# Kernel optimization log

Hardware: AMD Instinct MI355X
Metric: run time of the kernel (lower is better)

The kernel has to match this reference:

```python
import jax, jax.numpy as jnp
import numpy as np

NUM_RADIAL = 8    # radial Gaussian shells
NUM_ANGULAR = 4   # l=0 (scalar) + l=1 (unit direction x,y,z)
MAX_R = 3.0       # max radius covered by radial basis
GAMMA = 8.0       # Gaussian sharpness ~ (NUM_RADIAL/MAX_R)^2
C_IN = 16
C_OUT = 16
EPS = 1e-12


def setup_inputs() -> dict:
    key = jax.random.key(0)
    k1, k2, k3 = jax.random.split(key, 3)
    features = jax.random.normal(k1, (4, 512, C_IN), dtype=jnp.float32)
    geometry = jax.random.normal(k2, (4, 512, 3), dtype=jnp.float32)
    # learned kernel weights mixing radial x angular basis into [out,in] channel map
    W = jax.random.normal(k3, (NUM_RADIAL, NUM_ANGULAR, C_OUT, C_IN), dtype=jnp.float32)
    W = W / np.float32(np.sqrt(NUM_RADIAL * NUM_ANGULAR * C_IN))
    return {"features": features, "geometry": geometry, "W": W, "n_norm": 512}


def _kernel_basis(rel):
    # rel: [z, a, b, 3] relative positions (r_b - r_a)
    d = jnp.sqrt(jnp.sum(rel * rel, axis=-1) + EPS)           # [z,a,b]
    unit = rel / d[..., None]                                  # [z,a,b,3]
    # angular basis: l=0 constant + l=1 unit vector -> [z,a,b,4]
    ang = jnp.concatenate([jnp.ones_like(d)[..., None], unit], axis=-1)
    centers = jnp.linspace(0.0, MAX_R, NUM_RADIAL, dtype=rel.dtype)
    rad = jnp.exp(-GAMMA * (d[..., None] - centers) ** 2)      # [z,a,b,R]
    return rad, ang


def reference(features, geometry, W, n_norm):
    # rb - ra with out_geometry = geometry (module default)
    rel = geometry[:, None, :, :] - geometry[:, :, None, :]    # [z,a,b,3]
    rad, ang = _kernel_basis(rel)
    # dense pairwise kernel [z,a,b,i,j] (this is the HBM-heavy intermediate)
    k = jnp.einsum('zabr,zabm,rmij->zabij', rad, ang, W)
    k = k * (1.0 / jnp.sqrt(jnp.asarray(n_norm, dtype=features.dtype)))
    # contract kernel with input features over neighbor b and in-channel j
    return jnp.einsum('zabij,zbj->zai', k, features)
```

## Files before the change

kernel.cpp:

```cpp
#include <hip/hip_runtime.h>
#include <hip/hip_fp16.h>

typedef _Float16 f16x8 __attribute__((ext_vector_type(8)));
typedef float    f32x4 __attribute__((ext_vector_type(4)));

#define S    512
#define CIN  16
#define COUT 16

static __device__ inline unsigned int pkrtz(float lo, float hi) {
    auto h = __builtin_amdgcn_cvt_pkrtz(lo, hi);
    return __builtin_bit_cast(unsigned int, h);
}

__global__ __launch_bounds__(256, 2)
void econv_mfma(const float* __restrict__ feat,
                const float* __restrict__ geom,
                const float* __restrict__ Wm,
                const int*   __restrict__ n_norm,
                float*       __restrict__ out)
{
    __shared__ float          Glds[S * 3];
    __shared__ unsigned short FtU[16 * S];
    __shared__ unsigned short BasU[4 * 32 * 128];

    const int t = threadIdx.x;
    const int z = blockIdx.x >> 7;
    const int a0 = (blockIdx.x & 127) << 2;
    const int w = t >> 6;
    const int l = t & 63;

    const float* gz = geom + z * S * 3;
    const float* fz = feat + z * S * CIN;

    for (int k = t; k < S * 3; k += 256) Glds[k] = gz[k];

    {
        const int j  = t & 15;
        const int b0 = (t >> 4) * 32;
        const int key = (j & 7) << 4;
        char* FtB = (char*)FtU;
#pragma unroll
        for (int bi = 0; bi < 32; bi += 2) {
            float f0 = fz[(b0 + bi) * CIN + j];
            float f1 = fz[(b0 + bi + 1) * CIN + j];
            *(unsigned int*)(FtB + j * 1024 + ((2 * (b0 + bi)) ^ key)) = pkrtz(f0, f1);
        }
    }
    __syncthreads();

    const int a = a0 + w;
    const float gax = Glds[3 * a], gay = Glds[3 * a + 1], gaz = Glds[3 * a + 2];

    char* BasB = (char*)(BasU + w * 32 * 128);
    char* FtB  = (char*)FtU;

    const int mrow = l & 15;
    const int g    = l >> 4;
    const int rkey = (mrow & 7) << 4;
    const int wbase = 4 * l;

    f32x4 acc0 = {0.f, 0.f, 0.f, 0.f};
    f32x4 acc1 = {0.f, 0.f, 0.f, 0.f};

    for (int c = 0; c < 4; ++c) {
        float v0[32];
        unsigned int pw[32];
        {
            const int b = c * 128 + 2 * l;
            float dx = Glds[3 * b] - gax, dy = Glds[3 * b + 1] - gay, dz = Glds[3 * b + 2] - gaz;
            float ss  = fmaf(dx, dx, fmaf(dy, dy, fmaf(dz, dz, 1e-12f)));
            float inv = rsqrtf(ss);
            float d   = ss * inv;
            float ux = dx * inv, uy = dy * inv, uz = dz * inv;
#pragma unroll
            for (int r = 0; r < 8; ++r) {
                float e   = d - (float)r * (3.0f / 7.0f);
                float rad = __expf(-8.0f * e * e);
                v0[4 * r]     = rad;
                v0[4 * r + 1] = rad * ux;
                v0[4 * r + 2] = rad * uy;
                v0[4 * r + 3] = rad * uz;
            }
        }
        {
            const int b = c * 128 + 2 * l + 1;
            float dx = Glds[3 * b] - gax, dy = Glds[3 * b + 1] - gay, dz = Glds[3 * b + 2] - gaz;
            float ss  = fmaf(dx, dx, fmaf(dy, dy, fmaf(dz, dz, 1e-12f)));
            float inv = rsqrtf(ss);
            float d   = ss * inv;
            float ux = dx * inv, uy = dy * inv, uz = dz * inv;
#pragma unroll
            for (int r = 0; r < 8; ++r) {
                float e   = d - (float)r * (3.0f / 7.0f);
                float rad = __expf(-8.0f * e * e);
                pw[4 * r]     = pkrtz(v0[4 * r],     rad);
                pw[4 * r + 1] = pkrtz(v0[4 * r + 1], rad * ux);
                pw[4 * r + 2] = pkrtz(v0[4 * r + 2], rad * uy);
                pw[4 * r + 3] = pkrtz(v0[4 * r + 3], rad * uz);
            }
        }
#pragma unroll
        for (int rm = 0; rm < 32; ++rm) {
            *(unsigned int*)(BasB + rm * 256 + (wbase ^ ((rm & 7) << 4))) = pw[rm];
        }

#pragma unroll
        for (int ks = 0; ks < 4; ++ks) {
            const int colb = 64 * ks + 16 * g;
            f16x8 A0 = *(f16x8*)(BasB + mrow * 256        + (colb ^ rkey));
            f16x8 A1 = *(f16x8*)(BasB + (mrow + 16) * 256 + (colb ^ rkey));
            f16x8 Bf = *(f16x8*)(FtB  + mrow * 1024 + ((c * 256 + colb) ^ rkey));
            acc0 = __builtin_amdgcn_mfma_f32_16x16x32_f16(A0, Bf, acc0, 0, 0, 0);
            acc1 = __builtin_amdgcn_mfma_f32_16x16x32_f16(A1, Bf, acc1, 0, 0, 0);
        }
    }

    float* Tl = (float*)BasB;
#pragma unroll
    for (int q = 0; q < 4; ++q) {
        Tl[(4 * g + q) * 16 + mrow]      = acc0[q];
        Tl[(16 + 4 * g + q) * 16 + mrow] = acc1[q];
    }

    float o = 0.f;
    const float* Wp = Wm + (g * 8) * COUT * CIN + mrow * CIN;
#pragma unroll
    for (int rr = 0; rr < 8; ++rr) {
        const float* Trow = Tl + (g * 8 + rr) * 16;
        const float* Wrow = Wp + rr * COUT * CIN;
#pragma unroll
        for (int j4 = 0; j4 < 4; ++j4) {
            f32x4 tv = *(const f32x4*)(Trow + 4 * j4);
            f32x4 wv = *(const f32x4*)(Wrow + 4 * j4);
            o = fmaf(tv[0], wv[0], o);
            o = fmaf(tv[1], wv[1], o);
            o = fmaf(tv[2], wv[2], o);
            o = fmaf(tv[3], wv[3], o);
        }
    }
    o += __shfl_xor(o, 16);
    o += __shfl_xor(o, 32);
    if (l < 16) {
        const float scale = rsqrtf((float)n_norm[0]);
        out[(z * S + a) * COUT + mrow] = o * scale;
    }
}

extern "C" void kernel_launch(void* const* d_in, const int* in_sizes, int n_in,
                              void* d_out, int out_size, void* d_ws, size_t ws_size,
                              hipStream_t stream) {
    const float* feat   = (const float*)d_in[0];
    const float* geomp  = (const float*)d_in[1];
    const float* Wm     = (const float*)d_in[2];
    const int*   n_norm = (const int*)d_in[3];
    float* outp = (float*)d_out;

    dim3 grid(512), block(256);
    econv_mfma<<<grid, block, 0, stream>>>(feat, geomp, Wm, n_norm, outp);
}
```

Before: 14.93 us.

## Split each atom's neighbor range across two waves and double the grid

```diff
diff --git a/kernel.cpp b/kernel.cpp
--- a/kernel.cpp
+++ b/kernel.cpp
@@ -13,7 +13,7 @@
     return __builtin_bit_cast(unsigned int, h);
 }
 
-__global__ __launch_bounds__(256, 2)
+__global__ __launch_bounds__(256, 4)
 void econv_mfma(const float* __restrict__ feat,
                 const float* __restrict__ geom,
                 const float* __restrict__ Wm,
@@ -22,18 +22,22 @@
 {
     __shared__ float          Glds[S * 3];
     __shared__ unsigned short FtU[16 * S];
-    __shared__ unsigned short BasU[4 * 32 * 128];
+    __shared__ unsigned short BasU[4 * 32 * 64];
 
     const int t = threadIdx.x;
-    const int z = blockIdx.x >> 7;
-    const int a0 = (blockIdx.x & 127) << 2;
+    const int z = blockIdx.x >> 8;
+    const int a0 = (blockIdx.x & 255) << 1;
     const int w = t >> 6;
     const int l = t & 63;
+    const int a_loc = w >> 1;
+    const int wh    = w & 1;
 
     const float* gz = geom + z * S * 3;
     const float* fz = feat + z * S * CIN;
 
-    for (int k = t; k < S * 3; k += 256) Glds[k] = gz[k];
+#pragma unroll
+    for (int k = 0; k < (S * 3) / 256; ++k)
+        Glds[k * 256 + t] = gz[k * 256 + t];
 
     {
         const int j  = t & 15;
@@ -49,68 +53,63 @@
     }
     __syncthreads();
 
-    const int a = a0 + w;
+    const int a = a0 + a_loc;
     const float gax = Glds[3 * a], gay = Glds[3 * a + 1], gaz = Glds[3 * a + 2];
 
-    char* BasB = (char*)(BasU + w * 32 * 128);
+    char* BasB = (char*)(BasU + w * 32 * 64);
     char* FtB  = (char*)FtU;
 
     const int mrow = l & 15;
     const int g    = l >> 4;
     const int rkey = (mrow & 7) << 4;
-    const int wbase = 4 * l;
+    const int s    = l & 31;
+    const int hh   = l >> 5;
 
     f32x4 acc0 = {0.f, 0.f, 0.f, 0.f};
     f32x4 acc1 = {0.f, 0.f, 0.f, 0.f};
 
     for (int c = 0; c < 4; ++c) {
-        float v0[32];
-        unsigned int pw[32];
-        {
-            const int b = c * 128 + 2 * l;
-            float dx = Glds[3 * b] - gax, dy = Glds[3 * b + 1] - gay, dz = Glds[3 * b + 2] - gaz;
-            float ss  = fmaf(dx, dx, fmaf(dy, dy, fmaf(dz, dz, 1e-12f)));
-            float inv = rsqrtf(ss);
-            float d   = ss * inv;
-            float ux = dx * inv, uy = dy * inv, uz = dz * inv;
+        const int bloc = wh * 256 + c * 64 + 2 * s;
+        const char* gp = (const char*)Glds + 12 * bloc;
+        float2 g01 = *(const float2*)(gp);
+        float2 g23 = *(const float2*)(gp + 8);
+        float2 g45 = *(const float2*)(gp + 16);
+
+        float dx0 = g01.x - gax, dy0 = g01.y - gay, dz0 = g23.x - gaz;
+        float dx1 = g23.y - gax, dy1 = g45.x - gay, dz1 = g45.y - gaz;
+        float ss0 = fmaf(dx0, dx0, fmaf(dy0, dy0, fmaf(dz0, dz0, 1e-12f)));
+        float ss1 = fmaf(dx1, dx1, fmaf(dy1, dy1, fmaf(dz1, dz1, 1e-12f)));
+        float inv0 = rsqrtf(ss0), inv1 = rsqrtf(ss1);
+        float dd0 = ss0 * inv0,  dd1 = ss1 * inv1;
+        float ux0 = dx0 * inv0, uy0 = dy0 * inv0, uz0 = dz0 * inv0;
+        float ux1 = dx1 * inv1, uy1 = dy1 * inv1, uz1 = dz1 * inv1;
+
+        unsigned int pw[16];
 #pragma unroll
-            for (int r = 0; r < 8; ++r) {
-                float e   = d - (float)r * (3.0f / 7.0f);
-                float rad = __expf(-8.0f * e * e);
-                v0[4 * r]     = rad;
-                v0[4 * r + 1] = rad * ux;
-                v0[4 * r + 2] = rad * uy;
-                v0[4 * r + 3] = rad * uz;
-            }
+        for (int rr = 0; rr < 4; ++rr) {
+            const float cen = (float)(4 * hh + rr) * (3.0f / 7.0f);
+            float e0 = dd0 - cen, e1 = dd1 - cen;
+            float rad0 = __expf(-8.0f * e0 * e0);
+            float rad1 = __expf(-8.0f * e1 * e1);
+            pw[4 * rr + 0] = pkrtz(rad0,       rad1);
+            pw[4 * rr + 1] = pkrtz(rad0 * ux0, rad1 * ux1);
+            pw[4 * rr + 2] = pkrtz(rad0 * uy0, rad1 * uy1);
+            pw[4 * rr + 3] = pkrtz(rad0 * uz0, rad1 * uz1);
         }
-        {
-            const int b = c * 128 + 2 * l + 1;
-            float dx = Glds[3 * b] - gax, dy = Glds[3 * b + 1] - gay, dz = Glds[3 * b + 2] - gaz;
-            float ss  = fmaf(dx, dx, fmaf(dy, dy, fmaf(dz, dz, 1e-12f)));
-            float inv = rsqrtf(ss);
-            float d   = ss * inv;
-            float ux = dx * inv, uy = dy * inv, uz = dz * inv;
+        const unsigned int wb = 4 * s;
 #pragma unroll
-            for (int r = 0; r < 8; ++r) {
-                float e   = d - (float)r * (3.0f / 7.0f);
-                float rad = __expf(-8.0f * e * e);
-                pw[4 * r]     = pkrtz(v0[4 * r],     rad);
-                pw[4 * r + 1] = pkrtz(v0[4 * r + 1], rad * ux);
-                pw[4 * r + 2] = pkrtz(v0[4 * r + 2], rad * uy);
-                pw[4 * r + 3] = pkrtz(v0[4 * r + 3], rad * uz);
-            }
-        }
-#pragma unroll
-        for (int rm = 0; rm < 32; ++rm) {
-            *(unsigned int*)(BasB + rm * 256 + (wbase ^ ((rm & 7) << 4))) = pw[rm];
+        for (int k = 0; k < 16; ++k) {
+            const int rm = hh * 16 + k;
+            *(unsigned int*)(BasB + rm * 128 + (wb ^ ((k & 7) << 4))) = pw[k];
         }
 
 #pragma unroll
-        for (int ks = 0; ks < 4; ++ks) {
+        for (int ks = 0; ks < 2; ++ks) {
             const int colb = 64 * ks + 16 * g;
-            f16x8 A0 = *(f16x8*)(BasB + mrow * 256        + (colb ^ rkey));
-            f16x8 A1 = *(f16x8*)(BasB + (mrow + 16) * 256 + (colb ^ rkey));
-            f16x8 Bf = *(f16x8*)(FtB  + mrow * 1024 + ((c * 256 + colb) ^ rkey));
+            f16x8 A0 = *(f16x8*)(BasB + mrow * 128        + (colb ^ rkey));
+            f16x8 A1 = *(f16x8*)(BasB + (mrow + 16) * 128 + (colb ^ rkey));
+            f16x8 Bf = *(f16x8*)(FtB + mrow * 1024 +
+                                 ((wh * 512 + c * 128 + colb) ^ rkey));
             acc0 = __builtin_amdgcn_mfma_f32_16x16x32_f16(A0, Bf, acc0, 0, 0, 0);
             acc1 = __builtin_amdgcn_mfma_f32_16x16x32_f16(A1, Bf, acc1, 0, 0, 0);
         }
@@ -122,28 +121,32 @@
         Tl[(4 * g + q) * 16 + mrow]      = acc0[q];
         Tl[(16 + 4 * g + q) * 16 + mrow] = acc1[q];
     }
+    __syncthreads();
 
-    float o = 0.f;
-    const float* Wp = Wm + (g * 8) * COUT * CIN + mrow * CIN;
+    if (wh == 0) {
+        const float* T0 = (const float*)((const char*)BasU + (2 * a_loc)     * 4096);
+        const float* T1 = (const float*)((const char*)BasU + (2 * a_loc + 1) * 4096);
+        float o = 0.f;
 #pragma unroll
-    for (int rr = 0; rr < 8; ++rr) {
-        const float* Trow = Tl + (g * 8 + rr) * 16;
-        const float* Wrow = Wp + rr * COUT * CIN;
+        for (int rr = 0; rr < 8; ++rr) {
+            const int row = g * 8 + rr;
 #pragma unroll
-        for (int j4 = 0; j4 < 4; ++j4) {
-            f32x4 tv = *(const f32x4*)(Trow + 4 * j4);
-            f32x4 wv = *(const f32x4*)(Wrow + 4 * j4);
-            o = fmaf(tv[0], wv[0], o);
-            o = fmaf(tv[1], wv[1], o);
-            o = fmaf(tv[2], wv[2], o);
-            o = fmaf(tv[3], wv[3], o);
+            for (int j4 = 0; j4 < 4; ++j4) {
+                f32x4 tv = *(const f32x4*)(T0 + row * 16 + 4 * j4) +
+                           *(const f32x4*)(T1 + row * 16 + 4 * j4);
+                f32x4 wv = *(const f32x4*)(Wm + row * 256 + mrow * 16 + 4 * j4);
+                o = fmaf(tv[0], wv[0], o);
+                o = fmaf(tv[1], wv[1], o);
+                o = fmaf(tv[2], wv[2], o);
+                o = fmaf(tv[3], wv[3], o);
+            }
         }
-    }
-    o += __shfl_xor(o, 16);
-    o += __shfl_xor(o, 32);
-    if (l < 16) {
-        const float scale = rsqrtf((float)n_norm[0]);
-        out[(z * S + a) * COUT + mrow] = o * scale;
+        o += __shfl_xor(o, 16);
+        o += __shfl_xor(o, 32);
+        if (l < 16) {
+            const float scale = rsqrtf((float)n_norm[0]);
+            out[(z * S + a) * COUT + mrow] = o * scale;
+        }
     }
 }
 
@@ -156,6 +159,6 @@
     const int*   n_norm = (const int*)d_in[3];
     float* outp = (float*)d_out;
 
-    dim3 grid(512), block(256);
+    dim3 grid(1024), block(256);
     econv_mfma<<<grid, block, 0, stream>>>(feat, geomp, Wm, n_norm, outp);
 }
```

After: 15.84 us. 1.06x slower.

## Pre-transpose features to fp16 in a separate kernel, read operands from global

Applied to the files above, without the earlier changes.

```diff
diff --git a/kernel.cpp b/kernel.cpp
--- a/kernel.cpp
+++ b/kernel.cpp
@@ -1,5 +1,4 @@
 #include <hip/hip_runtime.h>
-#include <hip/hip_fp16.h>
 
 typedef _Float16 f16x8 __attribute__((ext_vector_type(8)));
 typedef float    f32x4 __attribute__((ext_vector_type(4)));
@@ -13,15 +12,26 @@
     return __builtin_bit_cast(unsigned int, h);
 }
 
+__global__ __launch_bounds__(256)
+void transpose_feat(const float* __restrict__ feat, unsigned short* __restrict__ ft)
+{
+    const int id = blockIdx.x * 256 + threadIdx.x;
+    const int bp = id & 255;
+    const int j  = (id >> 8) & 15;
+    const int z  = id >> 12;
+    const float* fz = feat + z * S * CIN;
+    float f0 = fz[(2 * bp)     * CIN + j];
+    float f1 = fz[(2 * bp + 1) * CIN + j];
+    *(unsigned int*)((char*)ft + z * 16384 + j * 1024 + 4 * bp) = pkrtz(f0, f1);
+}
+
 __global__ __launch_bounds__(256, 2)
-void econv_mfma(const float* __restrict__ feat,
-                const float* __restrict__ geom,
+void econv_mfma(const float* __restrict__ geom,
+                const unsigned short* __restrict__ ft,
                 const float* __restrict__ Wm,
                 const int*   __restrict__ n_norm,
                 float*       __restrict__ out)
 {
-    __shared__ float          Glds[S * 3];
-    __shared__ unsigned short FtU[16 * S];
     __shared__ unsigned short BasU[4 * 32 * 128];
 
     const int t = threadIdx.x;
@@ -29,80 +39,54 @@
     const int a0 = (blockIdx.x & 127) << 2;
     const int w = t >> 6;
     const int l = t & 63;
+    const int a = a0 + w;
 
     const float* gz = geom + z * S * 3;
-    const float* fz = feat + z * S * CIN;
+    const char*  Fg = (const char*)ft + z * 16384;
 
-    for (int k = t; k < S * 3; k += 256) Glds[k] = gz[k];
+    const float gax = gz[3 * a], gay = gz[3 * a + 1], gaz = gz[3 * a + 2];
 
-    {
-        const int j  = t & 15;
-        const int b0 = (t >> 4) * 32;
-        const int key = (j & 7) << 4;
-        char* FtB = (char*)FtU;
-#pragma unroll
-        for (int bi = 0; bi < 32; bi += 2) {
-            float f0 = fz[(b0 + bi) * CIN + j];
-            float f1 = fz[(b0 + bi + 1) * CIN + j];
-            *(unsigned int*)(FtB + j * 1024 + ((2 * (b0 + bi)) ^ key)) = pkrtz(f0, f1);
-        }
-    }
-    __syncthreads();
-
-    const int a = a0 + w;
-    const float gax = Glds[3 * a], gay = Glds[3 * a + 1], gaz = Glds[3 * a + 2];
-
-    char* BasB = (char*)(BasU + w * 32 * 128);
-    char* FtB  = (char*)FtU;
-
+    char* BasB = (char*)BasU + w * 8192;
     const int mrow = l & 15;
     const int g    = l >> 4;
     const int rkey = (mrow & 7) << 4;
-    const int wbase = 4 * l;
+    const unsigned int wb = 4 * l;
 
     f32x4 acc0 = {0.f, 0.f, 0.f, 0.f};
     f32x4 acc1 = {0.f, 0.f, 0.f, 0.f};
 
+#pragma unroll
     for (int c = 0; c < 4; ++c) {
-        float v0[32];
+        const int b = c * 128 + 2 * l;
+        const float* gp = gz + 3 * b;
+        float2 q0 = *(const float2*)(gp);
+        float2 q1 = *(const float2*)(gp + 2);
+        float2 q2 = *(const float2*)(gp + 4);
+
+        float dx0 = q0.x - gax, dy0 = q0.y - gay, dz0 = q1.x - gaz;
+        float dx1 = q1.y - gax, dy1 = q2.x - gay, dz1 = q2.y - gaz;
+        float ss0 = fmaf(dx0, dx0, fmaf(dy0, dy0, fmaf(dz0, dz0, 1e-12f)));
+        float ss1 = fmaf(dx1, dx1, fmaf(dy1, dy1, fmaf(dz1, dz1, 1e-12f)));
+        float inv0 = rsqrtf(ss0), inv1 = rsqrtf(ss1);
+        float dd0 = ss0 * inv0,  dd1 = ss1 * inv1;
+        float ux0 = dx0 * inv0, uy0 = dy0 * inv0, uz0 = dz0 * inv0;
+        float ux1 = dx1 * inv1, uy1 = dy1 * inv1, uz1 = dz1 * inv1;
+
         unsigned int pw[32];
-        {
-            const int b = c * 128 + 2 * l;
-            float dx = Glds[3 * b] - gax, dy = Glds[3 * b + 1] - gay, dz = Glds[3 * b + 2] - gaz;
-            float ss  = fmaf(dx, dx, fmaf(dy, dy, fmaf(dz, dz, 1e-12f)));
-            float inv = rsqrtf(ss);
-            float d   = ss * inv;
-            float ux = dx * inv, uy = dy * inv, uz = dz * inv;
 #pragma unroll
-            for (int r = 0; r < 8; ++r) {
-                float e   = d - (float)r * (3.0f / 7.0f);
-                float rad = __expf(-8.0f * e * e);
-                v0[4 * r]     = rad;
-                v0[4 * r + 1] = rad * ux;
-                v0[4 * r + 2] = rad * uy;
-                v0[4 * r + 3] = rad * uz;
-            }
-        }
-        {
-            const int b = c * 128 + 2 * l + 1;
-            float dx = Glds[3 * b] - gax, dy = Glds[3 * b + 1] - gay, dz = Glds[3 * b + 2] - gaz;
-            float ss  = fmaf(dx, dx, fmaf(dy, dy, fmaf(dz, dz, 1e-12f)));
-            float inv = rsqrtf(ss);
-            float d   = ss * inv;
-            float ux = dx * inv, uy = dy * inv, uz = dz * inv;
-#pragma unroll
-            for (int r = 0; r < 8; ++r) {
-                float e   = d - (float)r * (3.0f / 7.0f);
-                float rad = __expf(-8.0f * e * e);
-                pw[4 * r]     = pkrtz(v0[4 * r],     rad);
-                pw[4 * r + 1] = pkrtz(v0[4 * r + 1], rad * ux);
-                pw[4 * r + 2] = pkrtz(v0[4 * r + 2], rad * uy);
-                pw[4 * r + 3] = pkrtz(v0[4 * r + 3], rad * uz);
-            }
+        for (int r = 0; r < 8; ++r) {
+            const float cen = (float)r * (3.0f / 7.0f);
+            float e0 = dd0 - cen, e1 = dd1 - cen;
+            float rad0 = __expf(-8.0f * e0 * e0);
+            float rad1 = __expf(-8.0f * e1 * e1);
+            pw[4 * r + 0] = pkrtz(rad0,       rad1);
+            pw[4 * r + 1] = pkrtz(rad0 * ux0, rad1 * ux1);
+            pw[4 * r + 2] = pkrtz(rad0 * uy0, rad1 * uy1);
+            pw[4 * r + 3] = pkrtz(rad0 * uz0, rad1 * uz1);
         }
 #pragma unroll
         for (int rm = 0; rm < 32; ++rm) {
-            *(unsigned int*)(BasB + rm * 256 + (wbase ^ ((rm & 7) << 4))) = pw[rm];
+            *(unsigned int*)(BasB + rm * 256 + (wb ^ ((rm & 7) << 4))) = pw[rm];
         }
 
 #pragma unroll
@@ -110,7 +94,7 @@
             const int colb = 64 * ks + 16 * g;
             f16x8 A0 = *(f16x8*)(BasB + mrow * 256        + (colb ^ rkey));
             f16x8 A1 = *(f16x8*)(BasB + (mrow + 16) * 256 + (colb ^ rkey));
-            f16x8 Bf = *(f16x8*)(FtB  + mrow * 1024 + ((c * 256 + colb) ^ rkey));
+            f16x8 Bf = *(const f16x8*)(Fg + mrow * 1024 + c * 256 + colb);
             acc0 = __builtin_amdgcn_mfma_f32_16x16x32_f16(A0, Bf, acc0, 0, 0, 0);
             acc1 = __builtin_amdgcn_mfma_f32_16x16x32_f16(A1, Bf, acc1, 0, 0, 0);
         }
@@ -124,15 +108,13 @@
     }
 
     float o = 0.f;
-    const float* Wp = Wm + (g * 8) * COUT * CIN + mrow * CIN;
 #pragma unroll
     for (int rr = 0; rr < 8; ++rr) {
-        const float* Trow = Tl + (g * 8 + rr) * 16;
-        const float* Wrow = Wp + rr * COUT * CIN;
+        const int row = g * 8 + rr;
 #pragma unroll
         for (int j4 = 0; j4 < 4; ++j4) {
-            f32x4 tv = *(const f32x4*)(Trow + 4 * j4);
-            f32x4 wv = *(const f32x4*)(Wrow + 4 * j4);
+            f32x4 tv = *(const f32x4*)(Tl + row * 16 + 4 * j4);
+            f32x4 wv = *(const f32x4*)(Wm + row * 256 + mrow * 16 + 4 * j4);
             o = fmaf(tv[0], wv[0], o);
             o = fmaf(tv[1], wv[1], o);
             o = fmaf(tv[2], wv[2], o);
@@ -155,7 +137,8 @@
     const float* Wm     = (const float*)d_in[2];
     const int*   n_norm = (const int*)d_in[3];
     float* outp = (float*)d_out;
+    unsigned short* ftp = (unsigned short*)d_ws;
 
-    dim3 grid(512), block(256);
-    econv_mfma<<<grid, block, 0, stream>>>(feat, geomp, Wm, n_norm, outp);
+    transpose_feat<<<dim3(64), dim3(256), 0, stream>>>(feat, ftp);
+    econv_mfma<<<dim3(512), dim3(256), 0, stream>>>(geomp, ftp, Wm, n_norm, outp);
 }
```

Result: slower. 19.55 us (+31.0%).
